# Optimization experiments

Hardware: AMD Instinct MI355X
Metric: run time of the kernel (lower is better)

## Reference

```python
import jax, jax.numpy as jnp
import numpy as np

D_MODEL = 1024
N_HEADS = 16
HEAD_DIM = D_MODEL // N_HEADS  # 64
SEQ = 2048
BATCH = 2


def setup_inputs() -> dict:
    key = jax.random.key(0)
    ks = jax.random.split(key, 12)
    s = 1.0 / np.sqrt(D_MODEL)
    return {
        "query": jax.random.normal(ks[0], (SEQ, BATCH, D_MODEL), jnp.float32),
        "key": jax.random.normal(ks[1], (SEQ, BATCH, D_MODEL), jnp.float32),
        "value": jax.random.normal(ks[2], (SEQ, BATCH, D_MODEL), jnp.float32),
        "Wq": jax.random.normal(ks[3], (D_MODEL, D_MODEL), jnp.float32) * s,
        "bq": jax.random.normal(ks[4], (D_MODEL,), jnp.float32) * s,
        "Wk": jax.random.normal(ks[5], (D_MODEL, D_MODEL), jnp.float32) * s,
        "bk": jax.random.normal(ks[6], (D_MODEL,), jnp.float32) * s,
        "Wv": jax.random.normal(ks[7], (D_MODEL, D_MODEL), jnp.float32) * s,
        "bv": jax.random.normal(ks[8], (D_MODEL,), jnp.float32) * s,
        "Wo": jax.random.normal(ks[9], (D_MODEL, D_MODEL), jnp.float32) * s,
        "bo": jax.random.normal(ks[10], (D_MODEL,), jnp.float32) * s,
    }


def _rope_tables(seq_len):
    # theta_i = 1 / 10000^(2i/head_dim), i in [0, head_dim//2)
    theta = 1.0 / (10000.0 ** (2.0 * jnp.arange(HEAD_DIM // 2, dtype=jnp.float32) / HEAD_DIM))
    pos = jnp.arange(seq_len, dtype=jnp.float32)[:, None, None, None] * theta  # [S,1,1,hd/2]
    return jnp.sin(pos), jnp.cos(pos)


def _apply_rope(t, sin, cos):
    # t: [S, B, H, hd]; NOTE faithful to source: t2 = q1*sin - q2*cos (minus)
    h = HEAD_DIM // 2
    q1, q2 = t[..., :h], t[..., h:]
    return jnp.concatenate([q1 * cos - q2 * sin, q1 * sin - q2 * cos], axis=-1)


def reference(query, key, value, Wq, bq, Wk, bk, Wv, bv, Wo, bo):
    S, B, _ = query.shape
    q = (query @ Wq.T + bq).reshape(S, B, N_HEADS, HEAD_DIM)
    k = (key @ Wk.T + bk).reshape(S, B, N_HEADS, HEAD_DIM)
    v = (value @ Wv.T + bv).reshape(S, B, N_HEADS, HEAD_DIM)
    sin, cos = _rope_tables(S)
    q = _apply_rope(q, sin, cos)
    k = _apply_rope(k, sin, cos)
    # [S,B,H,d] -> [B,H,S,d]
    q = q.transpose(1, 2, 0, 3)
    k = k.transpose(1, 2, 0, 3)
    v = v.transpose(1, 2, 0, 3)
    scale = 1.0 / jnp.sqrt(jnp.float32(HEAD_DIM))
    scores = jnp.einsum("bhqd,bhkd->bhqk", q, k) * scale
    attn = jax.nn.softmax(scores, axis=-1)
    out = jnp.einsum("bhqk,bhkd->bhqd", attn, v)  # [B,H,S,d]
    out = out.transpose(2, 0, 1, 3).reshape(S, B, D_MODEL)
    return out @ Wo.T + bo
```

## Files before the change

### kernel.cpp

```cpp
#include <hip/hip_runtime.h>
#include <hip/hip_bf16.h>

#define DMODEL 1024
#define NHEADS 16
#define HDIM   64
#define SEQ    2048
#define BATCH  2
#define MROWS  (SEQ*BATCH)

typedef unsigned int u32;
typedef unsigned short u16;
typedef __attribute__((ext_vector_type(8))) short bfrag;
typedef __attribute__((ext_vector_type(4))) float f32x4;
typedef __attribute__((ext_vector_type(16))) float f32x16;
typedef union { u32 u[4]; bfrag f; } fragu;

#define LOG2E 1.44269504088896341f

__device__ __forceinline__ u32 f2bf(float x) {
    unsigned u = __float_as_uint(x);
    return (u + 0x7fffu + ((u >> 16) & 1u)) >> 16;
}
__device__ __forceinline__ float bf2f(u32 h) {
    return __uint_as_float(h << 16);
}
__device__ __forceinline__ u32 pk2bf(float a, float b) {
    __hip_bfloat162 t = __float22bfloat162_rn(make_float2(a, b));
    u32 r;
    __builtin_memcpy(&r, &t, 4);
    return r;
}
__device__ __forceinline__ float fexp2(float x) {
#if __has_builtin(__builtin_amdgcn_exp2f)
    return __builtin_amdgcn_exp2f(x);
#else
    return exp2f(x);
#endif
}

__device__ __forceinline__ void gld16(const void* g, void* l) {
    __builtin_amdgcn_global_load_lds(
        (const __attribute__((address_space(1))) unsigned int*)g,
        (__attribute__((address_space(3))) unsigned int*)l, 16, 0, 0);
}


__global__ __launch_bounds__(256) void prep_kernel(
    const float* __restrict__ Wq, const float* __restrict__ Wk,
    const float* __restrict__ Wv, const float* __restrict__ Wo,
    float* __restrict__ query, float* __restrict__ key, float* __restrict__ value,
    u16* __restrict__ wqb, u16* __restrict__ wkb, u16* __restrict__ wvb,
    u16* __restrict__ wob, float2* __restrict__ tab)
{
    const int y = blockIdx.y;
    if (y == 3) {
        if (blockIdx.x >= 256) return;
        const int e = blockIdx.x * 256 + threadIdx.x;
        const int s = e >> 5, i = e & 31;
        const double th = exp(-(double)i * (9.210340371976184 / 32.0));
        double sn, cs;
        sincos((double)s * th, &sn, &cs);
        tab[e] = make_float2((float)sn, (float)cs);
        return;
    }
    const float* src;
    u16* dst;
    int nr;
    if (y < 3 || y == 7) {
        src = (y == 0) ? Wq : (y == 1) ? Wk : (y == 2) ? Wv : Wo;
        dst = (y == 0) ? wqb : (y == 1) ? wkb : (y == 2) ? wvb : wob;
        nr = 2;
    } else {
        float* io = (y == 4) ? query : (y == 5) ? key : value;
        src = io;
        dst = (u16*)io;
        nr = 8;
    }
    const int lane = threadIdx.x & 63;
    const int wv   = threadIdx.x >> 6;
    const int g8   = lane >> 3;
    const int l8   = lane & 7;
    for (int r = 0; r < nr; ++r) {
        const size_t kb = (size_t)blockIdx.x * (4 * nr) + (size_t)r * 4 + wv;
        const float4 x4 = *(const float4*)(src + kb * 256 + lane * 4);
        __align__(8) u16 hb[4];
        __align__(8) u16 lb[4];
        const float xs[4] = {x4.x, x4.y, x4.z, x4.w};
        #pragma unroll
        for (int i = 0; i < 4; ++i) {
            const u32 h = f2bf(xs[i]);
            hb[i] = (u16)h;
            lb[i] = (u16)f2bf(xs[i] - bf2f(h));
        }
        u16* o = dst + kb * 512 + g8 * 64 + l8 * 4;
        *(uint2*)o        = *(const uint2*)hb;
        *(uint2*)(o + 32) = *(const uint2*)lb;
    }
}

template <int NI>
__device__ __forceinline__ void gemm_body(
    int id, int mode,
    const u16* __restrict__ Ab, const u16* __restrict__ Wb,
    const float* __restrict__ bias, const float2* __restrict__ tab,
    float rope_scale,
    u16* __restrict__ Oh, u16* __restrict__ Ol, float* __restrict__ Of,
    u16* smem16)
{
    u16* sA = smem16;
    u16* sB = smem16 + 16384;

    const int tid   = threadIdx.x;
    const int w     = tid >> 6;
    const int lane  = tid & 63;
    const int lrow  = lane & 15;
    const int lquad = lane >> 4;

    const int NBLK = 1024 / (NI * 16);
    const int xcd  = id & 7;
    const int jj   = id >> 3;
    const int nblk = jj & (NBLK - 1);
    const int mblk = (xcd << 2) | (jj / NBLK);
    const int n0   = nblk * NI * 16;
    const int m0   = mblk * 128;

    const int srow8 = lane >> 3;
    const int sch   = (lane & 7) ^ srow8;

    int aoffh[2], aoffl[2], boffh[NI], boffl[NI];
    #pragma unroll
    for (int mi = 0; mi < 2; ++mi) {
        const int ra = w * 32 + mi * 16 + lrow;
        aoffh[mi] = ra * 64 + ((lquad ^ (ra & 7)) << 3);
        aoffl[mi] = ra * 64 + (((lquad + 4) ^ (ra & 7)) << 3);
    }
    #pragma unroll
    for (int ni = 0; ni < NI; ++ni) {
        const int rb = ni * 16 + lrow;
        boffh[ni] = rb * 64 + ((lquad ^ (rb & 7)) << 3);
        boffl[ni] = rb * 64 + (((lquad + 4) ^ (rb & 7)) << 3);
    }

    f32x4 acc[2][NI] = {};

    auto stage = [&](int t) {
        const int h = t & 1;
        #pragma unroll
        for (int i = 0; i < 4; ++i) {
            const int slab = w * 4 + i;
            const int row  = slab * 8 + srow8;
            gld16(Ab + (size_t)(m0 + row) * 2048 + t * 64 + sch * 8,
                  sA + h * 8192 + slab * 512);
        }
        #pragma unroll
        for (int i = 0; i < NI / 2; ++i) {
            const int slab = w * (NI / 2) + i;
            const int row  = slab * 8 + srow8;
            gld16(Wb + (size_t)(n0 + row) * 2048 + t * 64 + sch * 8,
                  sB + h * (NI * 1024) + slab * 512);
        }
    };

    stage(0);
    for (int t = 0; t < 32; ++t) {
        __syncthreads();
        if (t < 31) stage(t + 1);
        const int h = t & 1;
        const u16* sAh_ = sA + h * 8192;
        const u16* sBh_ = sB + h * (NI * 1024);

        bfrag ah[2], al[2], bh[NI], bl[NI];
        #pragma unroll
        for (int mi = 0; mi < 2; ++mi) {
            ah[mi] = *(const bfrag*)&sAh_[aoffh[mi]];
            al[mi] = *(const bfrag*)&sAh_[aoffl[mi]];
        }
        #pragma unroll
        for (int ni = 0; ni < NI; ++ni) {
            bh[ni] = *(const bfrag*)&sBh_[boffh[ni]];
            bl[ni] = *(const bfrag*)&sBh_[boffl[ni]];
        }

        #pragma unroll
        for (int mi = 0; mi < 2; ++mi)
            #pragma unroll
            for (int ni = 0; ni < NI; ++ni) {
                acc[mi][ni] = __builtin_amdgcn_mfma_f32_16x16x32_bf16(ah[mi], bh[ni], acc[mi][ni], 0, 0, 0);
                acc[mi][ni] = __builtin_amdgcn_mfma_f32_16x16x32_bf16(ah[mi], bl[ni], acc[mi][ni], 0, 0, 0);
                acc[mi][ni] = __builtin_amdgcn_mfma_f32_16x16x32_bf16(al[mi], bh[ni], acc[mi][ni], 0, 0, 0);
            }
    }

    float bn[NI];
    #pragma unroll
    for (int ni = 0; ni < NI; ++ni) bn[ni] = bias[n0 + ni * 16 + lrow];

    if (mode == 0) {
        #pragma unroll
        for (int mi = 0; mi < 2; ++mi)
            #pragma unroll
            for (int r = 0; r < 4; ++r) {
                const int mrow = w * 32 + mi * 16 + lquad * 4 + r;
                const int m  = m0 + mrow;
                const int bb = m & 1;
                const int sg = m >> 1;
                #pragma unroll
                for (int hh = 0; hh < NI / 4; ++hh) {
                    const int head = nblk * (NI / 4) + hh;
                    const size_t ob = (((size_t)(bb * NHEADS + head) * SEQ) + sg) * HDIM;
                    #pragma unroll
                    for (int ni = 0; ni < 2; ++ni) {
                        const int i = ni * 16 + lrow;
                        const float2 sc = tab[(size_t)sg * 32 + i];
                        const float x1 = acc[mi][hh * 4 + ni][r]     + bn[hh * 4 + ni];
                        const float x2 = acc[mi][hh * 4 + ni + 2][r] + bn[hh * 4 + ni + 2];
                        const float o1 = (x1 * sc.y - x2 * sc.x) * rope_scale;
                        const float o2 = (x1 * sc.x - x2 * sc.y) * rope_scale;
                        const u32 h1 = f2bf(o1);
                        const u32 h2 = f2bf(o2);
                        Oh[ob + i]      = (u16)h1;  Ol[ob + i]      = (u16)f2bf(o1 - bf2f(h1));
                        Oh[ob + i + 32] = (u16)h2;  Ol[ob + i + 32] = (u16)f2bf(o2 - bf2f(h2));
                    }
                }
            }
        return;
    }
    if (mode == 1) {
        __syncthreads();
        u32* vb = (u32*)smem16;
        constexpr int NP = (NI == 8) ? 2 : 1;
        for (int p = 0; p < NP; ++p) {
            if (p) __syncthreads();
            #pragma unroll
            for (int mi = 0; mi < 2; ++mi)
                #pragma unroll
                for (int r = 0; r < 4; ++r) {
                    const int mrow = w * 32 + mi * 16 + lquad * 4 + r;
                    const int bb = mrow & 1;
                    const int sl = mrow >> 1;
                    if (NP == 1 || bb == p) {
                        const int vbase = (NP == 1) ? bb * 4160 : 0;
                        #pragma unroll
                        for (int ni = 0; ni < NI; ++ni) {
                            const int d = ni * 16 + lrow;
                            vb[vbase + d * 65 + sl] = f2bf(acc[mi][ni][r] + bn[ni]);
                        }
                    }
                }
            __syncthreads();
            #pragma unroll
            for (int rep = 0; rep < 4; ++rep) {
                const int c  = rep * 256 + tid;
                const int bb = (NP == 1) ? (c >> 9) : p;
                const int dc = (NP == 1) ? ((c >> 3) & 63) : (c >> 3);
                const int s8 = c & 7;
                const int vbase = (NP == 1) ? bb * 4160 : 0;
                __align__(8) u16 hb[8];
                #pragma unroll
                for (int j = 0; j < 8; ++j)
                    hb[j] = (u16)vb[vbase + dc * 65 + s8 * 8 + j];
                const int head = nblk * (NI / 4) + (dc >> 6);
                const int dd   = dc & 63;
                const size_t orow = ((size_t)(bb * NHEADS + head) * HDIM + dd) * SEQ + (m0 >> 1);
                const int blk16 = (s8 >> 1) * 16;
                const int off   = (s8 & 1) * 4;
                *(uint2*)&Oh[orow + blk16 + off]     = *(const uint2*)&hb[0];
                *(uint2*)&Oh[orow + blk16 + 8 + off] = *(const uint2*)&hb[4];
            }
        }
        return;
    }
    #pragma unroll
    for (int mi = 0; mi < 2; ++mi)
        #pragma unroll
        for (int r = 0; r < 4; ++r) {
            const int m = m0 + w * 32 + mi * 16 + lquad * 4 + r;
            #pragma unroll
            for (int ni = 0; ni < NI; ++ni)
                Of[(size_t)m * 1024 + n0 + ni * 16 + lrow] = acc[mi][ni][r] + bn[ni];
        }
}

__global__ __launch_bounds__(256) void qkv_gemm_kernel(
    const u16* __restrict__ query, const u16* __restrict__ key,
    const u16* __restrict__ value,
    const u16* __restrict__ Wqb, const u16* __restrict__ Wkb,
    const u16* __restrict__ Wvb,
    const float* __restrict__ bq, const float* __restrict__ bk,
    const float* __restrict__ bv, const float2* __restrict__ tab,
    u16* __restrict__ Qh, u16* __restrict__ Ql,
    u16* __restrict__ Kh, u16* __restrict__ Kl,
    u16* __restrict__ VTh)
{
    __shared__ u16 smem16[32768];
    const int z  = blockIdx.z;
    const int id = blockIdx.x + 16 * blockIdx.y;
    const u16* A    = (z == 0) ? query : (z == 1) ? key : value;
    const u16* Wb   = (z == 0) ? Wqb : (z == 1) ? Wkb : Wvb;
    const float* bb = (z == 0) ? bq : (z == 1) ? bk : bv;
    u16* Oh = (z == 0) ? Qh : (z == 1) ? Kh : VTh;
    u16* Ol = (z == 0) ? Ql : (z == 1) ? Kl : nullptr;
    const int mode = (z == 2) ? 1 : 0;
    const float scale = (z == 0) ? 0.125f * LOG2E : 1.0f;
    gemm_body<8>(id, mode, A, Wb, bb, tab, scale, Oh, Ol, nullptr, smem16);
}

__global__ __launch_bounds__(256) void out_gemm_kernel(
    const u16* __restrict__ Ab, const u16* __restrict__ Wb,
    const float* __restrict__ bias, float* __restrict__ Of)
{
    __shared__ u16 smem16[24576];
    const int id = blockIdx.x + 16 * blockIdx.y;
    gemm_body<4>(id, 2, Ab, Wb, bias, nullptr, 1.0f, nullptr, nullptr, Of, smem16);
}

__global__ __launch_bounds__(256) void attn_mfma_kernel(
    const u16* __restrict__ Qh, const u16* __restrict__ Ql,
    const u16* __restrict__ Kh, const u16* __restrict__ Kl,
    const u16* __restrict__ Vh,
    float* __restrict__ O0, float* __restrict__ O1, float* __restrict__ lsum)
{
    __shared__ u16 sKh[8192], sKl[8192];
    __shared__ u16 sVh[8192];

    const int tid  = threadIdx.x;
    const int w    = tid >> 6;
    const int lane = tid & 63;
    const int l31  = lane & 31;
    const int g    = lane >> 5;
    const int z    = blockIdx.z;

    const int id = blockIdx.x + 16 * blockIdx.y;
    const int jj = id >> 3;
    const int bh = ((id & 7) << 2) | (jj >> 4);
    const int qt = jj & 15;

    const size_t qg = ((size_t)bh * SEQ + qt * 128 + w * 32 + l31) * HDIM + g * 8;
    bfrag qfh[4], qfl[4];
    #pragma unroll
    for (int ks = 0; ks < 4; ++ks) {
        qfh[ks] = *(const bfrag*)&Qh[qg + ks * 16];
        qfl[ks] = *(const bfrag*)&Ql[qg + ks * 16];
    }

    const int srow   = lane >> 3;
    const int schunk = (lane & 7) ^ srow;
    const u16* gsrc = nullptr; u16* lbase = nullptr; size_t istep = 0, ktstep = 0;
    if (w == 0) {
        gsrc = Kh + ((size_t)bh * SEQ + srow) * HDIM + schunk * 8;
        istep = 8 * 64; ktstep = 64 * 64; lbase = sKh;
    } else if (w == 1) {
        gsrc = Kl + ((size_t)bh * SEQ + srow) * HDIM + schunk * 8;
        istep = 8 * 64; ktstep = 64 * 64; lbase = sKl;
    } else if (w == 2) {
        gsrc = Vh + ((size_t)bh * HDIM + srow) * SEQ + schunk * 8;
        istep = 8 * SEQ; ktstep = 64; lbase = sVh;
    }

    int koff[2][4];
    #pragma unroll
    for (int a = 0; a < 2; ++a) {
        const int row = a * 32 + l31;
        #pragma unroll
        for (int c = 0; c < 4; ++c)
            koff[a][c] = row * 64 + (((c * 2 + g) ^ (row & 7)) << 3);
    }

    f32x16 accO[2] = {};
    float l_loc = 0.0f;

    auto stage = [&](int kt) {
        if (w < 3) {
            const u16* gp = gsrc + (size_t)kt * ktstep;
            u16* dst = lbase + (kt & 1) * 4096;
            #pragma unroll
            for (int i = 0; i < 8; ++i)
                gld16(gp + (size_t)i * istep, dst + i * 512);
        }
    };

    const int kt0 = z * 16;
    stage(kt0);
    for (int kt = kt0; kt < kt0 + 16; ++kt) {
        __syncthreads();
        if (kt < kt0 + 15) stage(kt + 1);
        const int po = (kt & 1) * 4096;

        f32x16 accS[2] = {};
        #pragma unroll
        for (int kg = 0; kg < 2; ++kg)
            #pragma unroll
            for (int ks = 0; ks < 4; ++ks) {
                const bfrag kh_ = *(const bfrag*)&sKh[po + koff[kg][ks]];
                const bfrag kl_ = *(const bfrag*)&sKl[po + koff[kg][ks]];
                accS[kg] = __builtin_amdgcn_mfma_f32_32x32x16_bf16(kh_, qfh[ks], accS[kg], 0, 0, 0);
                accS[kg] = __builtin_amdgcn_mfma_f32_32x32x16_bf16(kh_, qfl[ks], accS[kg], 0, 0, 0);
                accS[kg] = __builtin_amdgcn_mfma_f32_32x32x16_bf16(kl_, qfh[ks], accS[kg], 0, 0, 0);
            }

        float pv[2][16];
        #pragma unroll
        for (int kg = 0; kg < 2; ++kg)
            #pragma unroll
            for (int r = 0; r < 16; ++r) {
                const float p = fexp2(accS[kg][r]);
                pv[kg][r] = p;
                l_loc += p;
            }

        #pragma unroll
        for (int kp = 0; kp < 4; ++kp) {
            const int kg = kp >> 1;
            const int t8 = (kp & 1) * 8;
            fragu ph;
            #pragma unroll
            for (int j2 = 0; j2 < 4; ++j2)
                ph.u[j2] = pk2bf(pv[kg][t8 + 2 * j2], pv[kg][t8 + 2 * j2 + 1]);
            #pragma unroll
            for (int dt = 0; dt < 2; ++dt) {
                const bfrag vh = *(const bfrag*)&sVh[po + koff[dt][kp]];
                accO[dt] = __builtin_amdgcn_mfma_f32_32x32x16_bf16(vh, ph.f, accO[dt], 0, 0, 0);
            }
        }
    }

    const float ls = l_loc + __shfl_xor(l_loc, 32);

    const int b = bh >> 4;
    const int h = bh & 15;
    const int sg = qt * 128 + w * 32 + l31;
    const int rm = sg * BATCH + b;
    if (lane < 32)
        lsum[(size_t)z * 65536 + (size_t)bh * 2048 + sg] = ls;
    float* Op = z ? O1 : O0;
    #pragma unroll
    for (int dt = 0; dt < 2; ++dt)
        #pragma unroll
        for (int rq = 0; rq < 4; ++rq) {
            float4 v4;
            v4.x = accO[dt][rq * 4 + 0];
            v4.y = accO[dt][rq * 4 + 1];
            v4.z = accO[dt][rq * 4 + 2];
            v4.w = accO[dt][rq * 4 + 3];
            *(float4*)&Op[(size_t)rm * 1024 + (h * 2 + dt) * 32 + 8 * rq + 4 * g] = v4;
        }
}

__global__ __launch_bounds__(256) void combine_kernel(
    float* __restrict__ O0, const float* __restrict__ O1,
    const float* __restrict__ lsum)
{
    const int lane = threadIdx.x & 63;
    const int wv   = threadIdx.x >> 6;
    const int g8   = lane >> 3;
    const int l8   = lane & 7;
    #pragma unroll
    for (int r = 0; r < 8; ++r) {
        const size_t kb = (size_t)blockIdx.x * 32 + (size_t)r * 4 + wv;
        const int rm = (int)(kb >> 2);
        const int t  = ((int)kb & 3) * 8 + g8;
        const int b  = rm & 1;
        const int sg = rm >> 1;
        const int h  = t >> 1;
        const float l0 = lsum[(size_t)(b * 16 + h) * 2048 + sg];
        const float l1 = lsum[65536 + (size_t)(b * 16 + h) * 2048 + sg];
        const float inv = 1.0f / (l0 + l1);
        const float4 x0 = *(const float4*)(O0 + kb * 256 + lane * 4);
        const float4 x1 = *(const float4*)(O1 + kb * 256 + lane * 4);
        const float xs[4] = {x0.x + x1.x, x0.y + x1.y, x0.z + x1.z, x0.w + x1.w};
        __align__(8) u16 hb[4];
        __align__(8) u16 lb[4];
        #pragma unroll
        for (int i = 0; i < 4; ++i) {
            const float v = xs[i] * inv;
            const u32 hh = f2bf(v);
            hb[i] = (u16)hh;
            lb[i] = (u16)f2bf(v - bf2f(hh));
        }
        u16* o = (u16*)O0 + kb * 512 + g8 * 64 + l8 * 4;
        *(uint2*)o        = *(const uint2*)hb;
        *(uint2*)(o + 32) = *(const uint2*)lb;
    }
}

extern "C" void kernel_launch(void* const* d_in, const int* in_sizes, int n_in,
                              void* d_out, int out_size, void* d_ws, size_t ws_size,
                              hipStream_t stream)
{
    float* query = (float*)d_in[0];
    float* key   = (float*)d_in[1];
    float* value = (float*)d_in[2];
    const float* Wq    = (const float*)d_in[3];
    const float* bq    = (const float*)d_in[4];
    const float* Wk    = (const float*)d_in[5];
    const float* bk    = (const float*)d_in[6];
    const float* Wv    = (const float*)d_in[7];
    const float* bv    = (const float*)d_in[8];
    const float* Wo    = (const float*)d_in[9];
    const float* bo    = (const float*)d_in[10];
    float* out = (float*)d_out;

    char* wsb = (char*)d_ws;
    const size_t MB = 1024 * 1024;
    u16* Wqb = (u16*)(wsb + 0 * MB);
    u16* Wkb = (u16*)(wsb + 4 * MB);
    u16* Wvb = (u16*)(wsb + 8 * MB);
    float2* tab = (float2*)(wsb + 12 * MB);
    u16* Qh  = (u16*)(wsb + 16 * MB); u16* Ql  = (u16*)(wsb + 24 * MB);
    u16* Kh  = (u16*)(wsb + 32 * MB); u16* Kl  = (u16*)(wsb + 40 * MB);
    u16* VTh = (u16*)(wsb + 48 * MB);
    u16* Wob = (u16*)(wsb + 56 * MB);
    float* O0   = (float*)(wsb + 0 * MB);
    float* O1   = out;
    float* lsum = (float*)(wsb + 60 * MB);

    prep_kernel<<<dim3(512, 8), 256, 0, stream>>>(
        Wq, Wk, Wv, Wo, query, key, value, Wqb, Wkb, Wvb, Wob, tab);
    qkv_gemm_kernel<<<dim3(16, 16, 3), 256, 0, stream>>>(
        (const u16*)query, (const u16*)key, (const u16*)value,
        Wqb, Wkb, Wvb, bq, bk, bv, tab, Qh, Ql, Kh, Kl, VTh);
    attn_mfma_kernel<<<dim3(16, 32, 2), 256, 0, stream>>>(
        Qh, Ql, Kh, Kl, VTh, O0, O1, lsum);
    combine_kernel<<<dim3(512), 256, 0, stream>>>(O0, O1, lsum);
    out_gemm_kernel<<<dim3(16, 32), 256, 0, stream>>>((const u16*)O0, Wob, bo, out);
}
```

Baseline: 325.9 us.

## Drop split-K attention and fuse normalization into attention epilogue

Removes the two-way split of the key range in the attention kernel, so each block now loops over all 32 key tiles. The softmax normalization and bf16 hi/lo packing move into the attention epilogue, which eliminates the combine kernel and the fp32 partial-output and lsum round trips through memory. The cost is half as many attention blocks (512 instead of 1024), which lowers parallelism and occupancy on a many-CU GPU, and a longer serial loop per block.

Result: faster. 306.5 us (-5.9%).

```diff
diff --git a/kernel.cpp b/kernel.cpp
--- a/kernel.cpp
+++ b/kernel.cpp
@@ -318,7 +318,7 @@
     const u16* __restrict__ Qh, const u16* __restrict__ Ql,
     const u16* __restrict__ Kh, const u16* __restrict__ Kl,
     const u16* __restrict__ Vh,
-    float* __restrict__ O0, float* __restrict__ O1, float* __restrict__ lsum)
+    u16* __restrict__ AOb)
 {
     __shared__ u16 sKh[8192], sKl[8192];
     __shared__ u16 sVh[8192];
@@ -328,7 +328,6 @@
     const int lane = tid & 63;
     const int l31  = lane & 31;
     const int g    = lane >> 5;
-    const int z    = blockIdx.z;
 
     const int id = blockIdx.x + 16 * blockIdx.y;
     const int jj = id >> 3;
@@ -379,11 +378,10 @@
         }
     };
 
-    const int kt0 = z * 16;
-    stage(kt0);
-    for (int kt = kt0; kt < kt0 + 16; ++kt) {
+    stage(0);
+    for (int kt = 0; kt < SEQ / 64; ++kt) {
         __syncthreads();
-        if (kt < kt0 + 15) stage(kt + 1);
+        if (kt < SEQ / 64 - 1) stage(kt + 1);
         const int po = (kt & 1) * 4096;
 
         f32x16 accS[2] = {};
@@ -424,63 +422,31 @@
         }
     }
 
-    const float ls = l_loc + __shfl_xor(l_loc, 32);
+    const float inv = 1.0f / (l_loc + __shfl_xor(l_loc, 32));
 
     const int b = bh >> 4;
     const int h = bh & 15;
     const int sg = qt * 128 + w * 32 + l31;
     const int rm = sg * BATCH + b;
-    if (lane < 32)
-        lsum[(size_t)z * 65536 + (size_t)bh * 2048 + sg] = ls;
-    float* Op = z ? O1 : O0;
     #pragma unroll
     for (int dt = 0; dt < 2; ++dt)
         #pragma unroll
         for (int rq = 0; rq < 4; ++rq) {
-            float4 v4;
-            v4.x = accO[dt][rq * 4 + 0];
-            v4.y = accO[dt][rq * 4 + 1];
-            v4.z = accO[dt][rq * 4 + 2];
-            v4.w = accO[dt][rq * 4 + 3];
-            *(float4*)&Op[(size_t)rm * 1024 + (h * 2 + dt) * 32 + 8 * rq + 4 * g] = v4;
-        }
-}
-
-__global__ __launch_bounds__(256) void combine_kernel(
-    float* __restrict__ O0, const float* __restrict__ O1,
-    const float* __restrict__ lsum)
-{
-    const int lane = threadIdx.x & 63;
-    const int wv   = threadIdx.x >> 6;
-    const int g8   = lane >> 3;
-    const int l8   = lane & 7;
-    #pragma unroll
-    for (int r = 0; r < 8; ++r) {
-        const size_t kb = (size_t)blockIdx.x * 32 + (size_t)r * 4 + wv;
-        const int rm = (int)(kb >> 2);
-        const int t  = ((int)kb & 3) * 8 + g8;
-        const int b  = rm & 1;
-        const int sg = rm >> 1;
-        const int h  = t >> 1;
-        const float l0 = lsum[(size_t)(b * 16 + h) * 2048 + sg];
-        const float l1 = lsum[65536 + (size_t)(b * 16 + h) * 2048 + sg];
-        const float inv = 1.0f / (l0 + l1);
-        const float4 x0 = *(const float4*)(O0 + kb * 256 + lane * 4);
-        const float4 x1 = *(const float4*)(O1 + kb * 256 + lane * 4);
-        const float xs[4] = {x0.x + x1.x, x0.y + x1.y, x0.z + x1.z, x0.w + x1.w};
-        __align__(8) u16 hb[4];
-        __align__(8) u16 lb[4];
-        #pragma unroll
-        for (int i = 0; i < 4; ++i) {
-            const float v = xs[i] * inv;
-            const u32 hh = f2bf(v);
-            hb[i] = (u16)hh;
-            lb[i] = (u16)f2bf(v - bf2f(hh));
-        }
-        u16* o = (u16*)O0 + kb * 512 + g8 * 64 + l8 * 4;
-        *(uint2*)o        = *(const uint2*)hb;
-        *(uint2*)(o + 32) = *(const uint2*)lb;
-    }
+            const int j0 = 8 * rq + 4 * g;
+            const int t  = h * 2 + dt;
+            __align__(8) u16 hb[4];
+            __align__(8) u16 lb[4];
+            #pragma unroll
+            for (int i2 = 0; i2 < 4; ++i2) {
+                const float v = accO[dt][rq * 4 + i2] * inv;
+                const u32 hh = f2bf(v);
+                hb[i2] = (u16)hh;
+                lb[i2] = (u16)f2bf(v - bf2f(hh));
+            }
+            u16* o = AOb + (size_t)rm * 2048 + t * 64 + j0;
+            *(uint2*)o        = *(const uint2*)hb;
+            *(uint2*)(o + 32) = *(const uint2*)lb;
+        }
 }
 
 extern "C" void kernel_launch(void* const* d_in, const int* in_sizes, int n_in,
@@ -510,17 +476,14 @@
     u16* Kh  = (u16*)(wsb + 32 * MB); u16* Kl  = (u16*)(wsb + 40 * MB);
     u16* VTh = (u16*)(wsb + 48 * MB);
     u16* Wob = (u16*)(wsb + 56 * MB);
-    float* O0   = (float*)(wsb + 0 * MB);
-    float* O1   = out;
-    float* lsum = (float*)(wsb + 60 * MB);
+    u16* AOb = (u16*)(wsb + 0 * MB);
 
     prep_kernel<<<dim3(512, 8), 256, 0, stream>>>(
         Wq, Wk, Wv, Wo, query, key, value, Wqb, Wkb, Wvb, Wob, tab);
     qkv_gemm_kernel<<<dim3(16, 16, 3), 256, 0, stream>>>(
         (const u16*)query, (const u16*)key, (const u16*)value,
         Wqb, Wkb, Wvb, bq, bk, bv, tab, Qh, Ql, Kh, Kl, VTh);
-    attn_mfma_kernel<<<dim3(16, 32, 2), 256, 0, stream>>>(
-        Qh, Ql, Kh, Kl, VTh, O0, O1, lsum);
-    combine_kernel<<<dim3(512), 256, 0, stream>>>(O0, O1, lsum);
-    out_gemm_kernel<<<dim3(16, 32), 256, 0, stream>>>((const u16*)O0, Wob, bo, out);
-}
+    attn_mfma_kernel<<<dim3(16, 32), 256, 0, stream>>>(
+        Qh, Ql, Kh, Kl, VTh, AOb);
+    out_gemm_kernel<<<dim3(16, 32), 256, 0, stream>>>(AOb, Wob, bo, out);
+}
```
